# Kernel optimization log

Measured on AMD Instinct MI355X. Metric: run time of the kernel, lower is better.

The kernel has to match this reference:

```python
import jax, jax.numpy as jnp
import numpy as np

A, B = 0.0, 1.0
U_LEFT, U_RIGHT = 0.0, 0.0
BOUNDARY_PENALTY = 10.0
N_POINTS = 32768
K_TEST = 1024  # sine test functions
LAYERS = [1, 256, 256, 256, 1]


def setup_inputs() -> dict:
    key = jax.random.key(0)
    ks = jax.random.split(key, 2 + len(LAYERS) - 1)
    # Gauss-Lobatto-like nodes: sorted points in (A, B)
    x = jnp.sort(jax.random.uniform(ks[0], (N_POINTS, 1), dtype=jnp.float32,
                                    minval=A, maxval=B), axis=0)
    # positive quadrature weights, scaled so sum(weights) ~ (B - A)
    weights = jax.random.uniform(ks[1], (N_POINTS,), dtype=jnp.float32) * (2.0 * (B - A) / N_POINTS)
    inp = {"x": x, "weights": weights}
    for i in range(len(LAYERS) - 1):
        fin, fout = LAYERS[i], LAYERS[i + 1]
        inp[f"W{i}"] = jax.random.normal(ks[2 + i], (fin, fout), dtype=jnp.float32) / np.sqrt(fin).astype(np.float32)
        inp[f"b{i}"] = jnp.zeros((fout,), dtype=jnp.float32)
    return inp


def _mlp(h, params):
    # tanh MLP, no activation on the last layer (matches MLP.forward)
    n = len(params)
    for i, (W, b) in enumerate(params):
        h = h @ W + b
        if i < n - 1:
            h = jnp.tanh(h)
    return h


def reference(x, weights, W0, b0, W1, b1, W2, b2, W3, b3):
    params = [(W0, b0), (W1, b1), (W2, b2), (W3, b3)]
    xf = x[:, 0]                                   # [N]

    u = _mlp(x, params)                            # [N, 1]

    # u_xx at every quadrature node via grad-of-grad, vmapped over points
    def u_scalar(xv):
        return _mlp(xv.reshape(1, 1), params)[0, 0]
    u_xx = jax.vmap(jax.grad(jax.grad(u_scalar)))(xf)   # [N]

    # analytic sine test functions v_k(x) = sin(pi k x), k = 1..K
    k = jnp.arange(1, K_TEST + 1, dtype=x.dtype)        # [K]
    test = jnp.sin(jnp.pi * k[:, None] * xf[None, :])   # [K, N]

    source = jnp.sin(jnp.pi * xf)                       # f(x) on the grid, [N]

    # batched quadrature: one matvec replaces the per-k Integrate loop
    Fk = test @ (weights * source)                      # [K]
    Rk = -(test @ (weights * u_xx))                     # [K]  (method 1: -int u_xx v_k)

    loss_interior = jnp.mean((Rk - Fk) ** 2)
    loss_boundary = 0.5 * BOUNDARY_PENALTY * (
        (u[0, 0] - U_LEFT) ** 2 + (u[-1, 0] - U_RIGHT) ** 2
    )
    return jnp.stack([loss_interior, loss_boundary])
```

## Files before the change

### kernel.cpp

```cpp
#include <hip/hip_runtime.h>
#include <cmath>

#define N_PTS 32768
#define HID   256
#define KTEST 1024
#define MB    32
#define RS    264
#define SKC   256
#define SKYB  (N_PTS / SKC)
#define SKGRID (4 * SKYB)
#define NBLK  (N_PTS / MB)

typedef float  f32x4  __attribute__((ext_vector_type(4)));
typedef short  s16x4  __attribute__((ext_vector_type(4)));
typedef short  s16x8  __attribute__((ext_vector_type(8)));
typedef __bf16 bf16x8 __attribute__((ext_vector_type(8)));


__device__ __forceinline__ float b2f(unsigned short s) {
    return __uint_as_float(((unsigned int)s) << 16);
}
__device__ __forceinline__ unsigned short cvt16(float x) {
    return __builtin_bit_cast(unsigned short, (__bf16)x);
}
__device__ __forceinline__ void split2(float x, unsigned short& hi, unsigned short& lo) {
    unsigned int b = __float_as_uint(x);
    hi = (unsigned short)(b >> 16);
    float hf = __uint_as_float(b & 0xFFFF0000u);
    lo = cvt16(x - hf);
}
__device__ __forceinline__ float fast_tanh(float z) {
    float e = __expf(2.0f * z);
    return 1.0f - 2.0f / (e + 1.0f);
}

__global__ __launch_bounds__(64) void wswz_kernel(
    const float* __restrict__ W1, const float* __restrict__ W2,
    unsigned short* __restrict__ Wh1, unsigned short* __restrict__ Wl1,
    unsigned short* __restrict__ Wh2, unsigned short* __restrict__ Wl2,
    unsigned int* __restrict__ counter)
{
    const int lane = threadIdx.x;
    const int t  = blockIdx.x;
    const int kc = blockIdx.y;
    const float* W = blockIdx.z ? W2 : W1;
    unsigned short* Wh = blockIdx.z ? Wh2 : Wh1;
    unsigned short* Wl = blockIdx.z ? Wl2 : Wl1;
    const int q = lane >> 4, ln = lane & 15;
    const int n = t * 16 + ln;
    const int kbase = kc * 32 + q * 8;

    s16x8 hv, lv;
    #pragma unroll
    for (int j = 0; j < 8; ++j) {
        unsigned short h, l;
        split2(W[(kbase + j) * HID + n], h, l);
        hv[j] = (short)h; lv[j] = (short)l;
    }
    const int out = ((t * 8 + kc) * 64 + lane) * 8;
    *(s16x8*)(Wh + out) = hv;
    *(s16x8*)(Wl + out) = lv;

    if (lane == 0 && t == 0 && kc == 0 && blockIdx.z == 0)
        *counter = 0u;
}

__global__ __launch_bounds__(512, 4) void mlp_kernel(
    const float* __restrict__ x, const float* __restrict__ wq,
    const float* __restrict__ W0, const float* __restrict__ b0,
    const float* __restrict__ b1v, const float* __restrict__ b2v,
    const float* __restrict__ W3, const float* __restrict__ b3,
    const unsigned short* __restrict__ W1h, const unsigned short* __restrict__ W1l,
    const unsigned short* __restrict__ W2h, const unsigned short* __restrict__ W2l,
    float* __restrict__ u_arr, float* __restrict__ d_arr,
    float* __restrict__ partF)
{
    __shared__ __align__(16) unsigned short Hb[3][MB][RS];
    __shared__ float sx_h[MB], sx_l[MB], sd[MB];

    const int tid = threadIdx.x;
    const int gp0 = blockIdx.x * MB;

    {
        const int m = tid & 31, seg = tid >> 5;
        const float xm = x[gp0 + m];
        #pragma unroll
        for (int jb = 0; jb < 4; ++jb) {
            s16x4 vy, vyp, vypp;
            #pragma unroll
            for (int jl = 0; jl < 4; ++jl) {
                const int j = seg * 16 + jb * 4 + jl;
                float w = W0[j];
                float z = fmaf(xm, w, b0[j]);
                float y = fast_tanh(z);
                float s = 1.0f - y * y;
                float yp = s * w;
                float ypp = -2.0f * y * yp * w;
                vy[jl]   = (short)cvt16(y);
                vyp[jl]  = (short)cvt16(yp);
                vypp[jl] = (short)cvt16(ypp);
            }
            const int j0 = seg * 16 + jb * 4;
            *(s16x4*)&Hb[0][m][j0] = vy;
            *(s16x4*)&Hb[1][m][j0] = vyp;
            *(s16x4*)&Hb[2][m][j0] = vypp;
        }
    }
    __syncthreads();

    const int lane = tid & 63, wv = tid >> 6;
    const int q = lane >> 4, ln = lane & 15;

    const int fragbase = (wv * 2) * 8 * 512 + lane * 8;

    for (int layer = 0; layer < 2; ++layer) {
        const unsigned short* __restrict__ WhW = (layer ? W2h : W1h) + fragbase;
        const unsigned short* __restrict__ WlW = (layer ? W2l : W1l) + fragbase;
        const float* __restrict__ bb = layer ? b2v : b1v;

        f32x4 acc[3][2][2];
        #pragma unroll
        for (int s = 0; s < 3; ++s)
            #pragma unroll
            for (int mf = 0; mf < 2; ++mf)
                #pragma unroll
                for (int nt = 0; nt < 2; ++nt)
                    acc[s][mf][nt] = (f32x4){0.f, 0.f, 0.f, 0.f};

        s16x8 bh[3][2], bl[3][2];
        #pragma unroll
        for (int p = 0; p < 2; ++p)
            #pragma unroll
            for (int nt = 0; nt < 2; ++nt) {
                bh[p][nt] = *(const s16x8*)(WhW + nt * 4096 + p * 512);
                bl[p][nt] = *(const s16x8*)(WlW + nt * 4096 + p * 512);
            }

        #pragma unroll
        for (int kc = 0; kc < 8; ++kc) {
            const int cur = kc % 3;
            const int pre = (kc + 2) % 3;
            if (kc < 6) {
                #pragma unroll
                for (int nt = 0; nt < 2; ++nt) {
                    const int off = nt * 4096 + (kc + 2) * 512;
                    bh[pre][nt] = *(const s16x8*)(WhW + off);
                    bl[pre][nt] = *(const s16x8*)(WlW + off);
                }
            }
            s16x8 av[3][2];
            #pragma unroll
            for (int s = 0; s < 3; ++s)
                #pragma unroll
                for (int mf = 0; mf < 2; ++mf)
                    av[s][mf] = *(const s16x8*)&Hb[s][mf * 16 + ln][kc * 32 + q * 8];
            #pragma unroll
            for (int s = 0; s < 3; ++s)
                #pragma unroll
                for (int mf = 0; mf < 2; ++mf)
                    #pragma unroll
                    for (int nt = 0; nt < 2; ++nt) {
                        acc[s][mf][nt] = __builtin_amdgcn_mfma_f32_16x16x32_bf16(
                            __builtin_bit_cast(bf16x8, av[s][mf]),
                            __builtin_bit_cast(bf16x8, bh[cur][nt]), acc[s][mf][nt], 0, 0, 0);
                        acc[s][mf][nt] = __builtin_amdgcn_mfma_f32_16x16x32_bf16(
                            __builtin_bit_cast(bf16x8, av[s][mf]),
                            __builtin_bit_cast(bf16x8, bl[cur][nt]), acc[s][mf][nt], 0, 0, 0);
                    }
        }
        __syncthreads();

        #pragma unroll
        for (int nt = 0; nt < 2; ++nt) {
            const int c = wv * 32 + nt * 16 + ln;
            const float bias = bb[c];
            #pragma unroll
            for (int mf = 0; mf < 2; ++mf) {
                #pragma unroll
                for (int i = 0; i < 4; ++i) {
                    const int r = mf * 16 + q * 4 + i;
                    float z   = acc[0][mf][nt][i] + bias;
                    float zp  = acc[1][mf][nt][i];
                    float zpp = acc[2][mf][nt][i];
                    float y  = fast_tanh(z);
                    float s  = 1.0f - y * y;
                    float yp = s * zp;
                    float ypp = fmaf(s, zpp, -2.0f * y * yp * zp);
                    Hb[0][r][c] = cvt16(y);
                    if (layer == 0) Hb[1][r][c] = cvt16(yp);
                    Hb[2][r][c] = cvt16(ypp);
                }
            }
        }
        __syncthreads();
    }

    float* psum = (float*)&Hb[1][0][0];
    {
        const int m = tid & 31, seg = tid >> 5;
        float su = 0.f, sx = 0.f;
        #pragma unroll
        for (int jj8 = 0; jj8 < 2; ++jj8) {
            const int j0 = seg * 16 + jj8 * 8;
            s16x8 vy = *(const s16x8*)&Hb[0][m][j0];
            s16x8 vx = *(const s16x8*)&Hb[2][m][j0];
            #pragma unroll
            for (int u = 0; u < 8; ++u) {
                float w3 = W3[j0 + u];
                su = fmaf(b2f((unsigned short)vy[u]), w3, su);
                sx = fmaf(b2f((unsigned short)vx[u]), w3, sx);
            }
        }
        psum[(0 * 16 + seg) * 32 + m] = su;
        psum[(1 * 16 + seg) * 32 + m] = sx;
    }
    __syncthreads();
    if (tid < MB) {
        float u = b3[0], uxx = 0.f;
        #pragma unroll
        for (int s2 = 0; s2 < 16; ++s2) {
            u   += psum[s2 * 32 + tid];
            uxx += psum[(16 + s2) * 32 + tid];
        }
        const int gp = gp0 + tid;
        u_arr[gp] = u;
        float xv = x[gp];
        float dv = -wq[gp] * (uxx + sinpif(xv));
        d_arr[gp] = dv;
        float xh = __uint_as_float(__float_as_uint(xv) & 0xFFFFF000u);
        sx_h[tid] = xh * 0.5f;
        sx_l[tid] = (xv - xh) * 0.5f;
        sd[tid]   = dv;
    }

    if (partF) {
        __syncthreads();
        const float k1 = (float)(tid + 1);
        const float k2 = (float)(tid + 513);
        float s1 = 0.f, s2 = 0.f;
        #pragma unroll 8
        for (int i = 0; i < MB; ++i) {
            float xh = sx_h[i], xl = sx_l[i], dv = sd[i];
            float f1 = __builtin_amdgcn_fractf(k1 * xh);
            float t1 = __builtin_amdgcn_fractf(fmaf(k1, xl, f1));
            s1 = fmaf(__builtin_amdgcn_sinf(t1), dv, s1);
            float f2 = __builtin_amdgcn_fractf(k2 * xh);
            float t2 = __builtin_amdgcn_fractf(fmaf(k2, xl, f2));
            s2 = fmaf(__builtin_amdgcn_sinf(t2), dv, s2);
        }
        partF[blockIdx.x * KTEST + tid]       = s1;
        partF[blockIdx.x * KTEST + tid + 512] = s2;
    }
}

__global__ __launch_bounds__(512) void reduce_kernel(
    const float* __restrict__ part, const float* __restrict__ u_arr,
    unsigned int* __restrict__ counter, float* __restrict__ red_g,
    float* __restrict__ out)
{
    __shared__ float sm[16][33];
    __shared__ int lastFlag;

    const int tid = threadIdx.x;
    const int kk = tid & 31;
    const int ch = tid >> 5;
    const int k = blockIdx.x * 32 + kk;

    const float* P = part + (ch << 6) * KTEST + k;
    float s = 0.f;
    #pragma unroll 8
    for (int b = 0; b < 64; ++b) s += P[b << 10];
    sm[ch][kk] = s;
    __syncthreads();

    if (tid < 32) {
        float t = 0.f;
        #pragma unroll
        for (int j = 0; j < 16; ++j) t += sm[j][kk];
        float sq = t * t;
        #pragma unroll
        for (int off = 16; off > 0; off >>= 1) sq += __shfl_down(sq, off, 64);
        if (kk == 0) red_g[blockIdx.x] = sq;
    }
    __threadfence();
    if (tid == 0)
        lastFlag = (atomicAdd(counter, 1u) == 31u);
    __syncthreads();
    if (!lastFlag) return;
    __threadfence();

    if (tid < 32) {
        float v = red_g[tid];
        #pragma unroll
        for (int off = 16; off > 0; off >>= 1) v += __shfl_down(v, off, 64);
        if (tid == 0) {
            out[0] = v * (1.0f / (float)KTEST);
            float u0 = u_arr[0], uN = u_arr[N_PTS - 1];
            out[1] = 5.0f * (u0 * u0 + uN * uN);
        }
    }
}

__global__ __launch_bounds__(256) void sk_loss_kernel(
    const float* __restrict__ x, const float* __restrict__ d_arr,
    const float* __restrict__ u_arr, float* __restrict__ part,
    unsigned int* __restrict__ counter, float* __restrict__ out)
{
    __shared__ float xs_h[SKC], xs_l[SKC], ds[SKC];
    __shared__ float red[4];
    __shared__ int lastFlag;

    const int tid = threadIdx.x;
    const int k = blockIdx.x * 256 + tid;
    const int i0 = blockIdx.y * SKC;

    {
        float xv = x[i0 + tid];
        float xh = __uint_as_float(__float_as_uint(xv) & 0xFFFFF000u);
        xs_h[tid] = xh * 0.5f;
        xs_l[tid] = (xv - xh) * 0.5f;
        ds[tid]   = d_arr[i0 + tid];
    }
    __syncthreads();

    const float kf = (float)(k + 1);
    float s = 0.f;
    #pragma unroll 8
    for (int i = 0; i < SKC; ++i) {
        float A = kf * xs_h[i];
        float f = __builtin_amdgcn_fractf(A);
        float t = __builtin_amdgcn_fractf(fmaf(kf, xs_l[i], f));
        s = fmaf(__builtin_amdgcn_sinf(t), ds[i], s);
    }
    part[blockIdx.y * KTEST + k] = s;

    __threadfence();
    if (tid == 0)
        lastFlag = (atomicAdd(counter, 1u) == (unsigned)(SKGRID - 1));
    __syncthreads();
    if (!lastFlag) return;
    __threadfence();

    float a0 = 0.f, a1 = 0.f, a2 = 0.f, a3 = 0.f;
    const float* P = part + tid * 4;
    for (int yb = 0; yb < SKYB; ++yb) {
        f32x4 v = *(const f32x4*)(P + yb * KTEST);
        a0 += v[0]; a1 += v[1]; a2 += v[2]; a3 += v[3];
    }
    float sq = a0 * a0 + a1 * a1 + a2 * a2 + a3 * a3;
    #pragma unroll
    for (int off = 32; off > 0; off >>= 1) sq += __shfl_down(sq, off, 64);
    if ((tid & 63) == 0) red[tid >> 6] = sq;
    __syncthreads();
    if (tid == 0) {
        float t = red[0] + red[1] + red[2] + red[3];
        out[0] = t * (1.0f / (float)KTEST);
        float u0 = u_arr[0], uN = u_arr[N_PTS - 1];
        out[1] = 5.0f * (u0 * u0 + uN * uN);
    }
}

extern "C" void kernel_launch(void* const* d_in, const int* in_sizes, int n_in,
                              void* d_out, int out_size, void* d_ws, size_t ws_size,
                              hipStream_t stream)
{
    const float* x  = (const float*)d_in[0];
    const float* wq = (const float*)d_in[1];
    const float* W0 = (const float*)d_in[2];
    const float* b0 = (const float*)d_in[3];
    const float* W1 = (const float*)d_in[4];
    const float* b1 = (const float*)d_in[5];
    const float* W2 = (const float*)d_in[6];
    const float* b2 = (const float*)d_in[7];
    const float* W3 = (const float*)d_in[8];
    const float* b3 = (const float*)d_in[9];
    float* out = (float*)d_out;

    float* ws    = (float*)d_ws;
    float* u_arr = ws;
    float* d_arr = ws + N_PTS;
    float* partS = ws + 2 * N_PTS;
    unsigned short* W1h = (unsigned short*)(ws + 2 * N_PTS + SKYB * KTEST);
    unsigned short* W1l = W1h + HID * HID;
    unsigned short* W2h = W1l + HID * HID;
    unsigned short* W2l = W2h + HID * HID;
    unsigned int* counter = (unsigned int*)(W2l + HID * HID);
    float* red_g = ws + 327696;
    float* partF = ws + 327744;
    const size_t need = (size_t)(327744 + NBLK * KTEST) * sizeof(float);
    const bool fused = ws_size >= need;

    wswz_kernel<<<dim3(16, 8, 2), 64, 0, stream>>>(W1, W2, W1h, W1l, W2h, W2l, counter);
    mlp_kernel<<<NBLK, 512, 0, stream>>>(x, wq, W0, b0, b1, b2, W3, b3,
                                         W1h, W1l, W2h, W2l, u_arr, d_arr,
                                         fused ? partF : nullptr);
    if (fused)
        reduce_kernel<<<32, 512, 0, stream>>>(partF, u_arr, counter, red_g, out);
    else
        sk_loss_kernel<<<dim3(4, SKYB), 256, 0, stream>>>(x, d_arr, u_arr, partS, counter, out);
}
```

Measured before the change: 131.3 us.

## Halve MLP block to 256 threads with four N-tiles per wave

Reduces the MLP kernel block from 512 to 256 threads, so each of four waves now covers 64 output columns (four 16-wide N tiles) instead of 32. The A-fragment loads from LDS are reused across more MFMAs and the triple-buffered B prefetch is replaced by direct per-kc loads. Every other phase (first layer, W3 reduction, sine projection) is rescaled to 256 threads. In exchange, per-thread work and accumulator registers double (launch bounds now 256,3), and losing the explicit prefetch may expose global load latency.

Measured after the change: 179.9 us. 37.1% more time.

```diff
diff --git a/kernel.cpp b/kernel.cpp
--- a/kernel.cpp
+++ b/kernel.cpp
@@ -65,7 +65,7 @@
         *counter = 0u;
 }
 
-__global__ __launch_bounds__(512, 4) void mlp_kernel(
+__global__ __launch_bounds__(256, 3) void mlp_kernel(
     const float* __restrict__ x, const float* __restrict__ wq,
     const float* __restrict__ W0, const float* __restrict__ b0,
     const float* __restrict__ b1v, const float* __restrict__ b2v,
@@ -85,11 +85,11 @@
         const int m = tid & 31, seg = tid >> 5;
         const float xm = x[gp0 + m];
         #pragma unroll
-        for (int jb = 0; jb < 4; ++jb) {
+        for (int jb = 0; jb < 8; ++jb) {
             s16x4 vy, vyp, vypp;
             #pragma unroll
             for (int jl = 0; jl < 4; ++jl) {
-                const int j = seg * 16 + jb * 4 + jl;
+                const int j = seg * 32 + jb * 4 + jl;
                 float w = W0[j];
                 float z = fmaf(xm, w, b0[j]);
                 float y = fast_tanh(z);
@@ -100,7 +100,7 @@
                 vyp[jl]  = (short)cvt16(yp);
                 vypp[jl] = (short)cvt16(ypp);
             }
-            const int j0 = seg * 16 + jb * 4;
+            const int j0 = seg * 32 + jb * 4;
             *(s16x4*)&Hb[0][m][j0] = vy;
             *(s16x4*)&Hb[1][m][j0] = vyp;
             *(s16x4*)&Hb[2][m][j0] = vypp;
@@ -111,68 +111,54 @@
     const int lane = tid & 63, wv = tid >> 6;
     const int q = lane >> 4, ln = lane & 15;
 
-    const int fragbase = (wv * 2) * 8 * 512 + lane * 8;
+    const int fragbase = (wv * 4) * 4096 + lane * 8;
 
     for (int layer = 0; layer < 2; ++layer) {
         const unsigned short* __restrict__ WhW = (layer ? W2h : W1h) + fragbase;
         const unsigned short* __restrict__ WlW = (layer ? W2l : W1l) + fragbase;
         const float* __restrict__ bb = layer ? b2v : b1v;
 
-        f32x4 acc[3][2][2];
+        f32x4 acc[3][2][4];
         #pragma unroll
         for (int s = 0; s < 3; ++s)
             #pragma unroll
             for (int mf = 0; mf < 2; ++mf)
                 #pragma unroll
-                for (int nt = 0; nt < 2; ++nt)
+                for (int nt = 0; nt < 4; ++nt)
                     acc[s][mf][nt] = (f32x4){0.f, 0.f, 0.f, 0.f};
 
-        s16x8 bh[3][2], bl[3][2];
-        #pragma unroll
-        for (int p = 0; p < 2; ++p)
-            #pragma unroll
-            for (int nt = 0; nt < 2; ++nt) {
-                bh[p][nt] = *(const s16x8*)(WhW + nt * 4096 + p * 512);
-                bl[p][nt] = *(const s16x8*)(WlW + nt * 4096 + p * 512);
-            }
-
-        #pragma unroll
         for (int kc = 0; kc < 8; ++kc) {
-            const int cur = kc % 3;
-            const int pre = (kc + 2) % 3;
-            if (kc < 6) {
+            s16x8 bh[4], bl[4];
+            #pragma unroll
+            for (int nt = 0; nt < 4; ++nt) {
+                const int off = nt * 4096 + kc * 512;
+                bh[nt] = *(const s16x8*)(WhW + off);
+                bl[nt] = *(const s16x8*)(WlW + off);
+            }
+            #pragma unroll
+            for (int mf = 0; mf < 2; ++mf) {
+                s16x8 av[3];
                 #pragma unroll
-                for (int nt = 0; nt < 2; ++nt) {
-                    const int off = nt * 4096 + (kc + 2) * 512;
-                    bh[pre][nt] = *(const s16x8*)(WhW + off);
-                    bl[pre][nt] = *(const s16x8*)(WlW + off);
-                }
-            }
-            s16x8 av[3][2];
-            #pragma unroll
-            for (int s = 0; s < 3; ++s)
+                for (int s = 0; s < 3; ++s)
+                    av[s] = *(const s16x8*)&Hb[s][mf * 16 + ln][kc * 32 + q * 8];
                 #pragma unroll
-                for (int mf = 0; mf < 2; ++mf)
-                    av[s][mf] = *(const s16x8*)&Hb[s][mf * 16 + ln][kc * 32 + q * 8];
-            #pragma unroll
-            for (int s = 0; s < 3; ++s)
-                #pragma unroll
-                for (int mf = 0; mf < 2; ++mf)
+                for (int s = 0; s < 3; ++s)
                     #pragma unroll
-                    for (int nt = 0; nt < 2; ++nt) {
+                    for (int nt = 0; nt < 4; ++nt) {
                         acc[s][mf][nt] = __builtin_amdgcn_mfma_f32_16x16x32_bf16(
-                            __builtin_bit_cast(bf16x8, av[s][mf]),
-                            __builtin_bit_cast(bf16x8, bh[cur][nt]), acc[s][mf][nt], 0, 0, 0);
+                            __builtin_bit_cast(bf16x8, av[s]),
+                            __builtin_bit_cast(bf16x8, bh[nt]), acc[s][mf][nt], 0, 0, 0);
                         acc[s][mf][nt] = __builtin_amdgcn_mfma_f32_16x16x32_bf16(
-                            __builtin_bit_cast(bf16x8, av[s][mf]),
-                            __builtin_bit_cast(bf16x8, bl[cur][nt]), acc[s][mf][nt], 0, 0, 0);
+                            __builtin_bit_cast(bf16x8, av[s]),
+                            __builtin_bit_cast(bf16x8, bl[nt]), acc[s][mf][nt], 0, 0, 0);
                     }
+            }
         }
         __syncthreads();
 
         #pragma unroll
-        for (int nt = 0; nt < 2; ++nt) {
-            const int c = wv * 32 + nt * 16 + ln;
+        for (int nt = 0; nt < 4; ++nt) {
+            const int c = (wv * 4 + nt) * 16 + ln;
             const float bias = bb[c];
             #pragma unroll
             for (int mf = 0; mf < 2; ++mf) {
@@ -200,8 +186,8 @@
         const int m = tid & 31, seg = tid >> 5;
         float su = 0.f, sx = 0.f;
         #pragma unroll
-        for (int jj8 = 0; jj8 < 2; ++jj8) {
-            const int j0 = seg * 16 + jj8 * 8;
+        for (int jj8 = 0; jj8 < 4; ++jj8) {
+            const int j0 = seg * 32 + jj8 * 8;
             s16x8 vy = *(const s16x8*)&Hb[0][m][j0];
             s16x8 vx = *(const s16x8*)&Hb[2][m][j0];
             #pragma unroll
@@ -211,16 +197,16 @@
                 sx = fmaf(b2f((unsigned short)vx[u]), w3, sx);
             }
         }
-        psum[(0 * 16 + seg) * 32 + m] = su;
-        psum[(1 * 16 + seg) * 32 + m] = sx;
+        psum[(0 * 8 + seg) * 32 + m] = su;
+        psum[(1 * 8 + seg) * 32 + m] = sx;
     }
     __syncthreads();
     if (tid < MB) {
         float u = b3[0], uxx = 0.f;
         #pragma unroll
-        for (int s2 = 0; s2 < 16; ++s2) {
+        for (int s2 = 0; s2 < 8; ++s2) {
             u   += psum[s2 * 32 + tid];
-            uxx += psum[(16 + s2) * 32 + tid];
+            uxx += psum[(8 + s2) * 32 + tid];
         }
         const int gp = gp0 + tid;
         u_arr[gp] = u;
@@ -236,20 +222,27 @@
     if (partF) {
         __syncthreads();
         const float k1 = (float)(tid + 1);
-        const float k2 = (float)(tid + 513);
-        float s1 = 0.f, s2 = 0.f;
-        #pragma unroll 8
+        const float k2 = (float)(tid + 257);
+        const float k3 = (float)(tid + 513);
+        const float k4 = (float)(tid + 769);
+        float s1 = 0.f, s2 = 0.f, s3 = 0.f, s4 = 0.f;
+        #pragma unroll 4
         for (int i = 0; i < MB; ++i) {
             float xh = sx_h[i], xl = sx_l[i], dv = sd[i];
-            float f1 = __builtin_amdgcn_fractf(k1 * xh);
-            float t1 = __builtin_amdgcn_fractf(fmaf(k1, xl, f1));
+            float t1 = __builtin_amdgcn_fractf(fmaf(k1, xl, __builtin_amdgcn_fractf(k1 * xh)));
             s1 = fmaf(__builtin_amdgcn_sinf(t1), dv, s1);
-            float f2 = __builtin_amdgcn_fractf(k2 * xh);
-            float t2 = __builtin_amdgcn_fractf(fmaf(k2, xl, f2));
+            float t2 = __builtin_amdgcn_fractf(fmaf(k2, xl, __builtin_amdgcn_fractf(k2 * xh)));
             s2 = fmaf(__builtin_amdgcn_sinf(t2), dv, s2);
-        }
-        partF[blockIdx.x * KTEST + tid]       = s1;
-        partF[blockIdx.x * KTEST + tid + 512] = s2;
+            float t3 = __builtin_amdgcn_fractf(fmaf(k3, xl, __builtin_amdgcn_fractf(k3 * xh)));
+            s3 = fmaf(__builtin_amdgcn_sinf(t3), dv, s3);
+            float t4 = __builtin_amdgcn_fractf(fmaf(k4, xl, __builtin_amdgcn_fractf(k4 * xh)));
+            s4 = fmaf(__builtin_amdgcn_sinf(t4), dv, s4);
+        }
+        float* row = partF + blockIdx.x * KTEST;
+        row[tid]       = s1;
+        row[tid + 256] = s2;
+        row[tid + 512] = s3;
+        row[tid + 768] = s4;
     }
 }
 
@@ -391,7 +384,7 @@
     const bool fused = ws_size >= need;
 
     wswz_kernel<<<dim3(16, 8, 2), 64, 0, stream>>>(W1, W2, W1h, W1l, W2h, W2l, counter);
-    mlp_kernel<<<NBLK, 512, 0, stream>>>(x, wq, W0, b0, b1, b2, W3, b3,
+    mlp_kernel<<<NBLK, 256, 0, stream>>>(x, wq, W0, b0, b1, b2, W3, b3,
                                          W1h, W1l, W2h, W2l, u_arr, d_arr,
                                          fused ? partF : nullptr);
     if (fused)
```
